# Performance work log

Measured on AMD Instinct MI355X. Metric: run time of the kernel, lower is better.

Reference implementation:

```python
import jax, jax.numpy as jnp
import numpy as np

AVG_FRAMES_PER_PHONE = 8.0


def setup_inputs() -> dict:
    key = jax.random.key(0)
    k1, k2, k3 = jax.random.split(key, 3)
    B, K, D, T = 16, 512, 256, 4096
    # positive durations averaging ~8 frames per phoneme
    durations = jax.random.uniform(k1, (B, K), dtype=jnp.float32) * (2.0 * AVG_FRAMES_PER_PHONE)
    phoneme = jax.random.normal(k2, (B, D, K), dtype=jnp.float32)
    frame = jax.random.normal(k3, (B, D, T), dtype=jnp.float32)
    return {"durations": durations, "phoneme": phoneme, "frame": frame}


def reference(durations, phoneme, frame):
    """Learnable duration upsampler (NaturalSpeech-style soft alignment).

    durations: (B, K) float frames per phoneme
    phoneme:   (B, D, K)
    frame:     (B, D, T)
    """
    T = frame.shape[-1]
    acc = jnp.cumsum(durations, axis=-1)                 # (B, K) end boundaries
    centers = acc - 0.5 * durations                      # (B, K) phoneme centers
    t = jnp.arange(T, dtype=durations.dtype) + 0.5       # (T,) frame centers
    # energy: negative squared distance frame-center -> phoneme-center
    energy = -((t[None, :, None] - centers[:, None, :]) ** 2)   # (B, T, K)
    w = jax.nn.softmax(energy, axis=-1)                  # soft alignment (B, T, K)
    upsampled = jnp.einsum("btk,bdk->bdt", w, phoneme)   # (B, D, T)
    return upsampled + frame
```

## Files before the change

### kernel.cpp

```cpp
#include <hip/hip_runtime.h>
#include <hip/hip_bf16.h>

#define BK 512
#define BD 256
#define BT 4096
#define TT 256
#define W  16
#define DSPLIT 8
#define ROWS (BD / DSPLIT)
#define SROWS 8
#define NSTAGE (ROWS / SROWS)

typedef __attribute__((address_space(1))) const float gfloat;
typedef __attribute__((address_space(3))) float lfloat;

__global__ __launch_bounds__(256)
void upsampler_kernel(const float* __restrict__ durations,
                      const float* __restrict__ phoneme,
                      const float* __restrict__ frame,
                      float* __restrict__ out)
{
    const int b   = blockIdx.x;
    const int tt  = blockIdx.y;
    const int ds  = blockIdx.z;
    const int tid = threadIdx.x;

    __shared__ float s_c[BK];
    __shared__ float s_ph[SROWS * BK];
    __shared__ float s_wsum[4];

    const float d0v = durations[b * BK + 2 * tid];
    const float d1v = durations[b * BK + 2 * tid + 1];
    float scan = d0v + d1v;
    #pragma unroll
    for (int off = 1; off < 64; off <<= 1) {
        float other = __shfl_up(scan, off, 64);
        if ((tid & 63) >= off) scan += other;
    }
    if ((tid & 63) == 63) s_wsum[tid >> 6] = scan;
    __syncthreads();
    float woff = 0.f;
    const int wv = tid >> 6;
    for (int i = 0; i < wv; ++i) woff += s_wsum[i];
    const float acc1 = woff + scan;
    s_c[2 * tid]     = (acc1 - d1v) - 0.5f * d0v;
    s_c[2 * tid + 1] = acc1 - 0.5f * d1v;
    __syncthreads();

    const float tc = (float)(tt * TT + tid) + 0.5f;

    int pos = 0;
    #pragma unroll
    for (int st = 256; st > 0; st >>= 1) {
        int np = pos + st;
        if (np <= BK && s_c[np - 1] < tc) pos = np;
    }
    int wstart = (pos - 7) & ~3;
    wstart = max(0, min(BK - W, wstart));

    float e[W];
    float m = -1e30f;
    #pragma unroll
    for (int j = 0; j < W; ++j) {
        float dd = tc - s_c[wstart + j];
        e[j] = -dd * dd;
        m = fmaxf(m, e[j]);
    }
    float sum = 0.f;
    #pragma unroll
    for (int j = 0; j < W; ++j) { e[j] = __expf(e[j] - m); sum += e[j]; }
    const float inv = 1.0f / sum;
    #pragma unroll
    for (int j = 0; j < W; ++j) e[j] *= inv;

    const int dlo = ds * ROWS;
    const float* phb  = phoneme + ((size_t)b * BD + dlo) * BK;
    const float* frb  = frame   + ((size_t)b * BD + dlo) * BT + (size_t)tt * TT;
    float*       outb = out     + ((size_t)b * BD + dlo) * BT + (size_t)tt * TT;

    for (int sg = 0; sg < NSTAGE; ++sg) {
        __syncthreads();
        const float* gsrc = phb + (size_t)sg * SROWS * BK;
        #pragma unroll
        for (int c = 0; c < 4; ++c) {
            const int off = (c * 256 + tid) * 4;
            __builtin_amdgcn_global_load_lds((gfloat*)(gsrc + off),
                                             (lfloat*)(s_ph + off), 16, 0, 0);
        }
        asm volatile("s_waitcnt vmcnt(0)" ::: "memory");
        __syncthreads();

        #pragma unroll
        for (int r = 0; r < SROWS; ++r) {
            const int d = sg * SROWS + r;
            const float4* sp4 = (const float4*)(s_ph + r * BK + wstart);
            float a0 = 0.f, a1 = 0.f, a2 = 0.f, a3 = 0.f;
            #pragma unroll
            for (int jj = 0; jj < W / 4; ++jj) {
                float4 p = sp4[jj];
                a0 += e[4 * jj + 0] * p.x;
                a1 += e[4 * jj + 1] * p.y;
                a2 += e[4 * jj + 2] * p.z;
                a3 += e[4 * jj + 3] * p.w;
            }
            const size_t idx = (size_t)d * BT + tid;
            outb[idx] = (a0 + a1) + (a2 + a3) + frb[idx];
        }
    }
}

extern "C" void kernel_launch(void* const* d_in, const int* in_sizes, int n_in,
                              void* d_out, int out_size, void* d_ws, size_t ws_size,
                              hipStream_t stream) {
    const float* durations = (const float*)d_in[0];
    const float* phoneme   = (const float*)d_in[1];
    const float* frame     = (const float*)d_in[2];
    float* out = (float*)d_out;

    dim3 grid(16, BT / TT, DSPLIT);
    upsampler_kernel<<<grid, 256, 0, stream>>>(durations, phoneme, frame, out);
}
```

Before: 147.7 us.

## Compute two frames per thread with shared phoneme window and packed FMA

Each thread now handles two adjacent frames, sharing one widened 20-wide phoneme window and each LDS read of phoneme values across both frames. Accumulation uses packed two-wide FMAs, and frame and output accesses become float2. The grid is reshaped to 512-frame spans and 16 D-splits, so each block stages fewer phoneme rows. The intent is to cut the LDS reads and the per-block phoneme staging and scan overhead per output. In exchange the softmax work per thread doubles, the window is wider, and register pressure rises.

```diff
diff --git a/kernel.cpp b/kernel.cpp
--- a/kernel.cpp
+++ b/kernel.cpp
@@ -4,15 +4,16 @@
 #define BK 512
 #define BD 256
 #define BT 4096
-#define TT 256
-#define W  16
-#define DSPLIT 8
+#define W  20
+#define DSPLIT 16
 #define ROWS (BD / DSPLIT)
 #define SROWS 8
 #define NSTAGE (ROWS / SROWS)
+#define TSPAN 512
 
 typedef __attribute__((address_space(1))) const float gfloat;
 typedef __attribute__((address_space(3))) float lfloat;
+typedef float v2f __attribute__((ext_vector_type(2)));
 
 __global__ __launch_bounds__(256)
 void upsampler_kernel(const float* __restrict__ durations,
@@ -47,36 +48,46 @@
     s_c[2 * tid + 1] = acc1 - 0.5f * d1v;
     __syncthreads();
 
-    const float tc = (float)(tt * TT + tid) + 0.5f;
+    const int   t0  = tt * TSPAN + 2 * tid;
+    const float tc0 = (float)t0 + 0.5f;
+    const float tc1 = (float)t0 + 1.5f;
+    const float tcm = (float)t0 + 1.0f;
 
     int pos = 0;
     #pragma unroll
     for (int st = 256; st > 0; st >>= 1) {
         int np = pos + st;
-        if (np <= BK && s_c[np - 1] < tc) pos = np;
+        if (np <= BK && s_c[np - 1] < tcm) pos = np;
     }
-    int wstart = (pos - 7) & ~3;
+    int wstart = (pos - 10) & ~3;
     wstart = max(0, min(BK - W, wstart));
 
-    float e[W];
-    float m = -1e30f;
+    float e0[W], e1[W];
+    float m0 = -1e30f, m1 = -1e30f;
     #pragma unroll
     for (int j = 0; j < W; ++j) {
-        float dd = tc - s_c[wstart + j];
-        e[j] = -dd * dd;
-        m = fmaxf(m, e[j]);
+        const float c = s_c[wstart + j];
+        float a = tc0 - c; e0[j] = -a * a; m0 = fmaxf(m0, e0[j]);
+        float bb = tc1 - c; e1[j] = -bb * bb; m1 = fmaxf(m1, e1[j]);
     }
-    float sum = 0.f;
+    float s0 = 0.f, s1 = 0.f;
     #pragma unroll
-    for (int j = 0; j < W; ++j) { e[j] = __expf(e[j] - m); sum += e[j]; }
-    const float inv = 1.0f / sum;
+    for (int j = 0; j < W; ++j) {
+        e0[j] = __expf(e0[j] - m0); s0 += e0[j];
+        e1[j] = __expf(e1[j] - m1); s1 += e1[j];
+    }
+    const float inv0 = 1.0f / s0, inv1 = 1.0f / s1;
+    v2f E0[W / 2], E1[W / 2];
     #pragma unroll
-    for (int j = 0; j < W; ++j) e[j] *= inv;
+    for (int j = 0; j < W / 2; ++j) {
+        E0[j] = (v2f){e0[2 * j] * inv0, e0[2 * j + 1] * inv0};
+        E1[j] = (v2f){e1[2 * j] * inv1, e1[2 * j + 1] * inv1};
+    }
 
     const int dlo = ds * ROWS;
     const float* phb  = phoneme + ((size_t)b * BD + dlo) * BK;
-    const float* frb  = frame   + ((size_t)b * BD + dlo) * BT + (size_t)tt * TT;
-    float*       outb = out     + ((size_t)b * BD + dlo) * BT + (size_t)tt * TT;
+    const float* frb  = frame   + ((size_t)b * BD + dlo) * BT + (size_t)tt * TSPAN + 2 * tid;
+    float*       outb = out     + ((size_t)b * BD + dlo) * BT + (size_t)tt * TSPAN + 2 * tid;
 
     for (int sg = 0; sg < NSTAGE; ++sg) {
         __syncthreads();
@@ -92,19 +103,24 @@
 
         #pragma unroll
         for (int r = 0; r < SROWS; ++r) {
+            const float4* sp4 = (const float4*)(s_ph + r * BK + wstart);
+            v2f a0 = (v2f){0.f, 0.f}, a1 = (v2f){0.f, 0.f};
+            #pragma unroll
+            for (int j = 0; j < W / 4; ++j) {
+                float4 p = sp4[j];
+                v2f lo = (v2f){p.x, p.y};
+                v2f hi = (v2f){p.z, p.w};
+                a0 = __builtin_elementwise_fma(E0[2 * j],     lo, a0);
+                a0 = __builtin_elementwise_fma(E0[2 * j + 1], hi, a0);
+                a1 = __builtin_elementwise_fma(E1[2 * j],     lo, a1);
+                a1 = __builtin_elementwise_fma(E1[2 * j + 1], hi, a1);
+            }
             const int d = sg * SROWS + r;
-            const float4* sp4 = (const float4*)(s_ph + r * BK + wstart);
-            float a0 = 0.f, a1 = 0.f, a2 = 0.f, a3 = 0.f;
-            #pragma unroll
-            for (int jj = 0; jj < W / 4; ++jj) {
-                float4 p = sp4[jj];
-                a0 += e[4 * jj + 0] * p.x;
-                a1 += e[4 * jj + 1] * p.y;
-                a2 += e[4 * jj + 2] * p.z;
-                a3 += e[4 * jj + 3] * p.w;
-            }
-            const size_t idx = (size_t)d * BT + tid;
-            outb[idx] = (a0 + a1) + (a2 + a3) + frb[idx];
+            const float2 fr = *(const float2*)(frb + (size_t)d * BT);
+            float2 o;
+            o.x = (a0.x + a0.y) + fr.x;
+            o.y = (a1.x + a1.y) + fr.y;
+            *(float2*)(outb + (size_t)d * BT) = o;
         }
     }
 }
@@ -117,6 +133,6 @@
     const float* frame     = (const float*)d_in[2];
     float* out = (float*)d_out;
 
-    dim3 grid(16, BT / TT, DSPLIT);
+    dim3 grid(16, BT / TSPAN, DSPLIT);
     upsampler_kernel<<<grid, 256, 0, stream>>>(durations, phoneme, frame, out);
 }
```

After: 131.7 us. 1.12x faster.
